# Optimization experiments

Measured on AMD Instinct MI355X. Metric: run time of the kernel, lower is better.

Reference implementation:

```python
import jax, jax.numpy as jnp
import numpy as np
import math

B, N, D, H, BS = 1, 2048, 1024, 16, 256  # batch, seq, d_model, heads, block_size


def setup_inputs() -> dict:
    key = jax.random.key(0)
    ks = jax.random.split(key, 8)
    s = 0.02  # init scale for projection weights
    return {
        "x": jax.random.normal(ks[0], (B, N, D), jnp.float32),
        "distance_bias": jax.random.uniform(ks[1], (N, N), dtype=jnp.float32),
        "Wq": jax.random.normal(ks[2], (D, D), jnp.float32) * s,
        "bq": jnp.zeros((D,), jnp.float32),
        "Wk": jax.random.normal(ks[3], (D, D), jnp.float32) * s,
        "bk": jnp.zeros((D,), jnp.float32),
        "Wv": jax.random.normal(ks[4], (D, D), jnp.float32) * s,
        "bv": jnp.zeros((D,), jnp.float32),
        "Wo": jax.random.normal(ks[5], (D, D), jnp.float32) * s,
        "bo": jnp.zeros((D,), jnp.float32),
    }


def reference(x, distance_bias, Wq, bq, Wk, bk, Wv, bv, Wo, bo):
    Bm, Nm, Dm = x.shape
    dk = Dm // H
    scale = 1.0 / math.sqrt(dk)
    nb = Nm // BS  # number of blocks along sequence

    def proj(W, b):
        # torch Linear: x @ W.T + b, then split heads -> [B, H, N, dk]
        return (x @ W.T + b).reshape(Bm, Nm, H, dk).transpose(0, 2, 1, 3)

    Q, K, V = proj(Wq, bq), proj(Wk, bk), proj(Wv, bv)

    # scores with toroidal bias subtracted (matches `scores - bias_block`)
    scores = jnp.einsum('bhqd,bhkd->bhqk', Q, K) * scale - distance_bias[None, None]
    # view as [B, H, n_qblk, BS, n_kblk, BS] and softmax PER (q-block, k-block)
    s6 = scores.reshape(Bm, H, nb, BS, nb, BS)
    w = jax.nn.softmax(s6, axis=-1)  # softmax over keys within each kv block

    Vb = V.reshape(Bm, H, nb, BS, dk)
    # sum over all kv blocks of (per-block softmax) @ V_block
    num = jnp.einsum('bhqsnk,bhnkd->bhqsd', w, Vb)  # [B,H,nb,BS,dk]
    # accumulated normalizer = sum of per-block softmax weights over all kv blocks
    norm = jnp.sum(w, axis=(4, 5))  # [B,H,nb,BS]
    O = num / (norm[..., None] + 1e-8)

    O = O.reshape(Bm, H, Nm, dk).transpose(0, 2, 1, 3).reshape(Bm, Nm, Dm)
    return O @ Wo.T + bo
```

## Files before the change

kernel.cpp:

```cpp
#include <hip/hip_runtime.h>
#include <hip/hip_fp16.h>

typedef _Float16 half8 __attribute__((ext_vector_type(8)));
typedef _Float16 half4v __attribute__((ext_vector_type(4)));
typedef float f32x4 __attribute__((ext_vector_type(4)));

#define NSEQ 2048
#define DMOD 1024
#define NHEAD 16
#define DK 64

#define GLOAD_LDS16(gp, lp) __builtin_amdgcn_global_load_lds(                 \
    (const __attribute__((address_space(1))) void*)(gp),                      \
    (__attribute__((address_space(3))) void*)(lp), 16, 0, 0)

#define WAIT_VM(n) (0xF70 | (n))


__global__ __launch_bounds__(256) void cast_pack(
    const float* __restrict__ x, const float* __restrict__ wq,
    const float* __restrict__ wk, const float* __restrict__ wv,
    const float* __restrict__ wo, const float* __restrict__ db,
    _Float16* __restrict__ dst, _Float16* __restrict__ bh)
{
    const int w = blockIdx.x * 4 + (threadIdx.x >> 6);
    const int ln = threadIdx.x & 63, m = ln & 15, qd = ln >> 4;
    if (w >= 12288) {
        const int loc = w - 12288;
        const float* p = db + (size_t)loc * 512 + ln * 8;
        float4 a = *(const float4*)p, b = *(const float4*)(p + 4);
        half8 h;
        h[0] = (_Float16)a.x; h[1] = (_Float16)a.y; h[2] = (_Float16)a.z; h[3] = (_Float16)a.w;
        h[4] = (_Float16)b.x; h[5] = (_Float16)b.y; h[6] = (_Float16)b.z; h[7] = (_Float16)b.w;
        *(half8*)(bh + (size_t)loc * 512 + ln * 8) = h;
        return;
    }
    const float* src; _Float16* d; int loc;
    if (w < 4096) { src = x; d = dst; loc = w; }
    else {
        const int w2 = w - 4096, mat = w2 >> 11;
        loc = w2 & 2047;
        src = mat == 0 ? wq : mat == 1 ? wk : mat == 2 ? wv : wo;
        d = dst + 2097152 + mat * 1048576;
    }
    const int st = loc >> 5, kc = loc & 31;
    const float* p = src + (size_t)(st * 16 + m) * 1024 + kc * 32 + qd * 8;
    float4 a = *(const float4*)p, b = *(const float4*)(p + 4);
    half8 h;
    h[0] = (_Float16)a.x; h[1] = (_Float16)a.y; h[2] = (_Float16)a.z; h[3] = (_Float16)a.w;
    h[4] = (_Float16)b.x; h[5] = (_Float16)b.y; h[6] = (_Float16)b.z; h[7] = (_Float16)b.w;
    *(half8*)(d + (size_t)(loc * 64 + ln) * 8) = h;
}

__global__ __launch_bounds__(256) void cvt_bias(
    const float* __restrict__ src, _Float16* __restrict__ dst)
{
    int i = (blockIdx.x * 256 + threadIdx.x) * 4;
    float4 v = *(const float4*)(src + i);
    half4v h;
    h[0] = (_Float16)v.x; h[1] = (_Float16)v.y;
    h[2] = (_Float16)v.z; h[3] = (_Float16)v.w;
    *(half4v*)(dst + i) = h;
}

template<int BM, int BN, int MODE>
__global__ __launch_bounds__(256) void tgemm(
    const _Float16* __restrict__ A, const _Float16* __restrict__ A2,
    const _Float16* __restrict__ W0, const _Float16* __restrict__ W1,
    const _Float16* __restrict__ W2,
    const float* __restrict__ b0, const float* __restrict__ b1,
    const float* __restrict__ b2,
    _Float16* __restrict__ oQ, _Float16* __restrict__ oK,
    _Float16* __restrict__ oV, float* __restrict__ oF)
{
    constexpr int MT = BM / 32, NT = BN / 32;
    constexpr int NA = BM / 64, NB = BN / 64;
    constexpr int SDMA = (MODE == 1 ? 2 * NA : NA) + NB;
    __shared__ _Float16 sA[3 * BM * 32];
    __shared__ _Float16 sA2[MODE == 1 ? 3 * BM * 32 : 1];
    __shared__ _Float16 sB[3 * BN * 32];
    const int tid = threadIdx.x, wv = tid >> 6, ln = tid & 63;
    const int m = ln & 15, qd = ln >> 4;
    const int row0 = blockIdx.x * BM;

    int sel = 0, colbase;
    const _Float16* W; const float* bias;
    if constexpr (MODE == 0) {
        sel = blockIdx.y >> 3;
        colbase = (blockIdx.y & 7) * BN;
        W = sel == 0 ? W0 : sel == 1 ? W1 : W2;
        bias = sel == 0 ? b0 : sel == 1 ? b1 : b2;
    } else {
        colbase = blockIdx.y * BN;
        W = W0; bias = b0;
    }
    const int wr = wv >> 1, wc = wv & 1;

    f32x4 acc[MT][NT];
#pragma unroll
    for (int i = 0; i < MT; ++i)
#pragma unroll
        for (int j = 0; j < NT; ++j) acc[i][j] = (f32x4){0.f, 0.f, 0.f, 0.f};

    auto stage = [&](int kc, int b) {
        _Float16* dA = sA + b * (BM * 32);
        _Float16* dB = sB + b * (BN * 32);
#pragma unroll
        for (int ra = 0; ra < NA; ++ra) {
            const int st = ra * 4 + wv;
            GLOAD_LDS16(A + ((size_t)((row0 >> 4) + st) * 32 + kc) * 512 + ln * 8,
                        dA + st * 512);
            if constexpr (MODE == 1) {
                _Float16* dA2 = sA2 + b * (BM * 32);
                GLOAD_LDS16(A2 + ((size_t)((row0 >> 4) + st) * 32 + kc) * 512 + ln * 8,
                            dA2 + st * 512);
            }
        }
#pragma unroll
        for (int rb = 0; rb < NB; ++rb) {
            const int st = rb * 4 + wv;
            GLOAD_LDS16(W + ((size_t)((colbase >> 4) + st) * 32 + kc) * 512 + ln * 8,
                        dB + st * 512);
        }
    };
    auto step = [&](int b) {
        const _Float16* cA = sA + b * (BM * 32);
        const _Float16* cB = sB + b * (BN * 32);
        half8 af[MT], bf[NT];
#pragma unroll
        for (int i = 0; i < MT; ++i) {
            const int off = ((wr * MT + i) * 64 + ln) * 8;
            if constexpr (MODE == 1) {
                const _Float16* cA2 = sA2 + b * (BM * 32);
                half8 xv = *(const half8*)(cA + off);
                half8 yv = *(const half8*)(cA2 + off);
                half8 f;
#pragma unroll
                for (int j = 0; j < 8; ++j)
                    f[j] = (_Float16)((float)xv[j] + (float)yv[j]);
                af[i] = f;
            } else {
                af[i] = *(const half8*)(cA + off);
            }
        }
#pragma unroll
        for (int j = 0; j < NT; ++j)
            bf[j] = *(const half8*)(cB + ((wc * NT + j) * 64 + ln) * 8);
#pragma unroll
        for (int i = 0; i < MT; ++i)
#pragma unroll
            for (int j = 0; j < NT; ++j)
                acc[i][j] = __builtin_amdgcn_mfma_f32_16x16x32_f16(af[i], bf[j], acc[i][j], 0, 0, 0);
    };

    stage(0, 0);
    stage(1, 1);
#pragma unroll
    for (int kc = 0; kc < 31; ++kc) {
        __builtin_amdgcn_s_waitcnt(WAIT_VM(SDMA));
        __builtin_amdgcn_s_barrier();
        if (kc < 30) stage(kc + 2, (kc + 2) % 3);
        step(kc % 3);
    }
    __builtin_amdgcn_s_waitcnt(WAIT_VM(0));
    __builtin_amdgcn_s_barrier();
    step(1);

#pragma unroll
    for (int j = 0; j < NT; ++j) {
        const int col = colbase + wc * (BN / 2) + j * 16 + m;
        const float bv = bias[col];
#pragma unroll
        for (int i = 0; i < MT; ++i) {
            const int crow0 = row0 + wr * (BM / 2) + i * 16 + qd * 4;
            if constexpr (MODE == 1) {
#pragma unroll
                for (int r = 0; r < 4; ++r)
                    oF[(size_t)(crow0 + r) * DMOD + col] = acc[i][j][r] + bv;
            } else {
                const int h = col >> 6, d = col & 63;
                if (sel == 0) {
#pragma unroll
                    for (int r = 0; r < 4; ++r)
                        oQ[h * (NSEQ * DK) + (crow0 + r) * DK + d] =
                            (_Float16)((acc[i][j][r] + bv) * 0.125f);
                } else if (sel == 1) {
#pragma unroll
                    for (int r = 0; r < 4; ++r) {
                        const int n = crow0 + r;
                        oK[(size_t)(((h * 16 + (n >> 7)) * 16
                                     + ((n >> 4) & 7) * 2 + (d >> 5)) * 64
                                    + (n & 15) + 16 * ((d >> 3) & 3)) * 8
                           + (d & 7)] = (_Float16)(acc[i][j][r] + bv);
                    }
                } else {
                    half4v hv;
#pragma unroll
                    for (int r = 0; r < 4; ++r) hv[r] = (_Float16)(acc[i][j][r] + bv);
                    const int n0 = crow0;
                    *(half4v*)(oV + (size_t)(((h * 16 + (n0 >> 7)) * 16
                                              + ((n0 >> 5) & 3) * 4 + ((d >> 4) & 3)) * 64
                                             + (d & 15) + 16 * ((n0 >> 3) & 3)) * 8
                               + (n0 & 7)) = hv;
                }
            }
        }
    }
}

__global__ __launch_bounds__(512, 4) void attn(
    const _Float16* __restrict__ Q, const _Float16* __restrict__ Kt,
    const _Float16* __restrict__ Vt, const _Float16* __restrict__ bias_h,
    _Float16* __restrict__ Op)
{
    __shared__ _Float16 sK[8192];
    __shared__ _Float16 sV[8192];
    __shared__ _Float16 sP[16384];
    const int tid = threadIdx.x, wv = tid >> 6, ln = tid & 63;
    const int m = ln & 15, qd = ln >> 4;
    const int h = blockIdx.x;
    const int q0 = blockIdx.y * 128 + wv * 16;
    const int kvb = blockIdx.z * 8;
    const _Float16* Qh = Q + h * (NSEQ * DK);
    const _Float16* Kh = Kt + h * (NSEQ * DK) + kvb * 8192;
    const _Float16* Vh = Vt + h * (NSEQ * DK) + kvb * 8192;
    const _Float16* brow = bias_h + (size_t)(q0 + m) * NSEQ + kvb * 128;

    half8 qf[2];
    qf[0] = *(const half8*)(Qh + (q0 + m) * DK + qd * 8);
    qf[1] = *(const half8*)(Qh + (q0 + m) * DK + 32 + qd * 8);

    f32x4 oacc[4], oU[4];
#pragma unroll
    for (int v = 0; v < 4; ++v) {
        oacc[v] = (f32x4){0.f, 0.f, 0.f, 0.f};
        oU[v]   = (f32x4){0.f, 0.f, 0.f, 0.f};
    }
    float bsum = 0.f;

    for (int ls = 0; ls < 8; ++ls) {
        if (ls) __syncthreads();
        GLOAD_LDS16(Kh + ls * 8192 + wv * 512 + ln * 8, sK + wv * 512);
        GLOAD_LDS16(Kh + ls * 8192 + (wv + 8) * 512 + ln * 8, sK + (wv + 8) * 512);
        GLOAD_LDS16(Vh + ls * 8192 + wv * 512 + ln * 8, sV + wv * 512);
        GLOAD_LDS16(Vh + ls * 8192 + (wv + 8) * 512 + ln * 8, sV + (wv + 8) * 512);
        half4v bcur[8];
#pragma unroll
        for (int t = 0; t < 8; ++t)
            bcur[t] = *(const half4v*)(brow + ls * 128 + t * 16 + qd * 4);
        __syncthreads();

#pragma unroll
        for (int t = 0; t < 8; ++t) {
            half8 kf0 = *(const half8*)(sK + ((t * 2 + 0) * 64 + ln) * 8);
            half8 kf1 = *(const half8*)(sK + ((t * 2 + 1) * 64 + ln) * 8);
            f32x4 s = {0.f, 0.f, 0.f, 0.f};
            s = __builtin_amdgcn_mfma_f32_16x16x32_f16(kf0, qf[0], s, 0, 0, 0);
            s = __builtin_amdgcn_mfma_f32_16x16x32_f16(kf1, qf[1], s, 0, 0, 0);
            float p0 = __expf(s[0] - (float)bcur[t][0]);
            float p1 = __expf(s[1] - (float)bcur[t][1]);
            float p2 = __expf(s[2] - (float)bcur[t][2]);
            float p3 = __expf(s[3] - (float)bcur[t][3]);
            bsum += (p0 + p1) + (p2 + p3);
            half4v ph;
            ph[0] = (_Float16)p0; ph[1] = (_Float16)p1;
            ph[2] = (_Float16)p2; ph[3] = (_Float16)p3;
            *(half4v*)(sP + wv * 2048 + (t >> 1) * 512
                       + (((t & 1) * 2 + (qd >> 1)) * 16 + m) * 8
                       + (qd & 1) * 4) = ph;
        }

#pragma unroll
        for (int kk = 0; kk < 4; ++kk) {
            half8 pa = *(const half8*)(sP + wv * 2048 + kk * 512 + ln * 8);
#pragma unroll
            for (int vt = 0; vt < 4; ++vt) {
                half8 vb = *(const half8*)(sV + ((kk * 4 + vt) * 64 + ln) * 8);
                oU[vt] = __builtin_amdgcn_mfma_f32_16x16x32_f16(pa, vb, oU[vt], 0, 0, 0);
            }
        }

        if (ls & 1) {
            float s2 = bsum;
            s2 += __shfl_xor(s2, 16, 64);
            s2 += __shfl_xor(s2, 32, 64);
            float inv = 1.0f / (8.0f * s2);
            float iv[4];
#pragma unroll
            for (int r = 0; r < 4; ++r) iv[r] = __shfl(inv, qd * 4 + r, 64);
#pragma unroll
            for (int vt = 0; vt < 4; ++vt) {
#pragma unroll
                for (int r = 0; r < 4; ++r) oacc[vt][r] += iv[r] * oU[vt][r];
                oU[vt] = (f32x4){0.f, 0.f, 0.f, 0.f};
            }
            bsum = 0.f;
        }
    }

    _Float16* Opz = Op + (size_t)blockIdx.z * 2097152;
    const int st = blockIdx.y * 8 + wv;
#pragma unroll
    for (int vt = 0; vt < 4; ++vt) {
        const int d = h * 64 + vt * 16 + m;
        _Float16* base = Opz + (size_t)(st * 32 + (d >> 5)) * 512
                         + ((d >> 3) & 3) * 128 + (d & 7);
#pragma unroll
        for (int r = 0; r < 4; ++r)
            base[(qd * 4 + r) * 8] = (_Float16)oacc[vt][r];
    }
}

extern "C" void kernel_launch(void* const* d_in, const int* in_sizes, int n_in,
                              void* d_out, int out_size, void* d_ws, size_t ws_size,
                              hipStream_t stream)
{
    const float* x  = (const float*)d_in[0];
    const float* db = (const float*)d_in[1];
    const float* Wq = (const float*)d_in[2];
    const float* bq = (const float*)d_in[3];
    const float* Wk = (const float*)d_in[4];
    const float* bk = (const float*)d_in[5];
    const float* Wv = (const float*)d_in[6];
    const float* bv = (const float*)d_in[7];
    const float* Wo = (const float*)d_in[8];
    const float* bo = (const float*)d_in[9];
    float* out = (float*)d_out;

    _Float16* ws  = (_Float16*)d_ws;
    _Float16* xh  = ws;
    _Float16* wqh = xh  + 2097152;
    _Float16* wkh = wqh + 1048576;
    _Float16* wvh = wkh + 1048576;
    _Float16* woh = wvh + 1048576;
    _Float16* Qb  = woh + 1048576;
    _Float16* Kb  = Qb  + 2097152;
    _Float16* Vtb = Kb  + 2097152;
    _Float16* Oh0 = Vtb + 2097152;
    _Float16* Oh1 = Oh0 + 2097152;

    const bool big_ws = ws_size >= (size_t)41943040;
    _Float16* bh = big_ws ? (Oh1 + 2097152) : ws;

    cast_pack<<<big_ws ? 5120 : 3072, 256, 0, stream>>>(
        x, Wq, Wk, Wv, Wo, db, xh, bh);

    tgemm<64, 128, 0><<<dim3(32, 24), 256, 0, stream>>>(
        xh, nullptr, wqh, wkh, wvh, bq, bk, bv, Qb, Kb, Vtb, nullptr);

    if (!big_ws)
        cvt_bias<<<4096, 256, 0, stream>>>(db, bh);

    attn<<<dim3(NHEAD, NSEQ / 128, 2), 512, 0, stream>>>(Qb, Kb, Vtb, bh, Oh0);

    tgemm<64, 128, 1><<<dim3(32, 8), 256, 0, stream>>>(
        Oh0, Oh1, woh, nullptr, nullptr, bo, nullptr, nullptr,
        nullptr, nullptr, nullptr, out);
}
```

Measured before the change: 180.5 us.

## Switch tgemm to double-buffered BK=64 stages and shrink output GEMM tile

The GEMM pipeline moves from a 3-stage ring of K=32 chunks to a 2-stage double buffer of K=64 chunks. This halves the number of barrier/wait iterations per K loop and doubles the MFMA work between syncs. The output projection GEMM also switches to a 64x64 tile on a 32x16 grid to put more blocks on the GPU. The trade-off is one less stage of prefetch depth, so load latency may be less well hidden, and the extra barrier per iteration adds some sync cost.

Measured after the change: 169.1 us. 1.07x faster.

```diff
diff --git a/kernel.cpp b/kernel.cpp
--- a/kernel.cpp
+++ b/kernel.cpp
@@ -63,7 +63,7 @@
     *(half4v*)(dst + i) = h;
 }
 
-template<int BM, int BN, int MODE>
+template<int BM, int BN, int BK, int MODE>
 __global__ __launch_bounds__(256) void tgemm(
     const _Float16* __restrict__ A, const _Float16* __restrict__ A2,
     const _Float16* __restrict__ W0, const _Float16* __restrict__ W1,
@@ -74,11 +74,13 @@
     _Float16* __restrict__ oV, float* __restrict__ oF)
 {
     constexpr int MT = BM / 32, NT = BN / 32;
-    constexpr int NA = BM / 64, NB = BN / 64;
-    constexpr int SDMA = (MODE == 1 ? 2 * NA : NA) + NB;
-    __shared__ _Float16 sA[3 * BM * 32];
-    __shared__ _Float16 sA2[MODE == 1 ? 3 * BM * 32 : 1];
-    __shared__ _Float16 sB[3 * BN * 32];
+    constexpr int KC = BK / 32;
+    constexpr int NSTEP = 1024 / BK;
+    constexpr int NAc = BM / 64, NBc = BN / 64;
+    constexpr int SDMA = KC * ((MODE == 1 ? 2 * NAc : NAc) + NBc);
+    __shared__ _Float16 sA[2 * BM * BK];
+    __shared__ _Float16 sA2[MODE == 1 ? 2 * BM * BK : 1];
+    __shared__ _Float16 sB[2 * BN * BK];
     const int tid = threadIdx.x, wv = tid >> 6, ln = tid & 63;
     const int m = ln & 15, qd = ln >> 4;
     const int row0 = blockIdx.x * BM;
@@ -102,69 +104,77 @@
 #pragma unroll
         for (int j = 0; j < NT; ++j) acc[i][j] = (f32x4){0.f, 0.f, 0.f, 0.f};
 
-    auto stage = [&](int kc, int b) {
-        _Float16* dA = sA + b * (BM * 32);
-        _Float16* dB = sB + b * (BN * 32);
-#pragma unroll
-        for (int ra = 0; ra < NA; ++ra) {
-            const int st = ra * 4 + wv;
-            GLOAD_LDS16(A + ((size_t)((row0 >> 4) + st) * 32 + kc) * 512 + ln * 8,
-                        dA + st * 512);
-            if constexpr (MODE == 1) {
-                _Float16* dA2 = sA2 + b * (BM * 32);
-                GLOAD_LDS16(A2 + ((size_t)((row0 >> 4) + st) * 32 + kc) * 512 + ln * 8,
-                            dA2 + st * 512);
-            }
-        }
-#pragma unroll
-        for (int rb = 0; rb < NB; ++rb) {
-            const int st = rb * 4 + wv;
-            GLOAD_LDS16(W + ((size_t)((colbase >> 4) + st) * 32 + kc) * 512 + ln * 8,
-                        dB + st * 512);
+    auto stage = [&](int s, int b) {
+        _Float16* dA = sA + b * (BM * BK);
+        _Float16* dB = sB + b * (BN * BK);
+#pragma unroll
+        for (int c = 0; c < KC; ++c) {
+            const int kc = s * KC + c;
+#pragma unroll
+            for (int ra = 0; ra < NAc; ++ra) {
+                const int st = ra * 4 + wv;
+                GLOAD_LDS16(A + ((size_t)((row0 >> 4) + st) * 32 + kc) * 512 + ln * 8,
+                            dA + (c * (BM / 16) + st) * 512);
+                if constexpr (MODE == 1) {
+                    _Float16* dA2 = sA2 + b * (BM * BK);
+                    GLOAD_LDS16(A2 + ((size_t)((row0 >> 4) + st) * 32 + kc) * 512 + ln * 8,
+                                dA2 + (c * (BM / 16) + st) * 512);
+                }
+            }
+#pragma unroll
+            for (int rb = 0; rb < NBc; ++rb) {
+                const int st = rb * 4 + wv;
+                GLOAD_LDS16(W + ((size_t)((colbase >> 4) + st) * 32 + kc) * 512 + ln * 8,
+                            dB + (c * (BN / 16) + st) * 512);
+            }
         }
     };
     auto step = [&](int b) {
-        const _Float16* cA = sA + b * (BM * 32);
-        const _Float16* cB = sB + b * (BN * 32);
-        half8 af[MT], bf[NT];
-#pragma unroll
-        for (int i = 0; i < MT; ++i) {
-            const int off = ((wr * MT + i) * 64 + ln) * 8;
-            if constexpr (MODE == 1) {
-                const _Float16* cA2 = sA2 + b * (BM * 32);
-                half8 xv = *(const half8*)(cA + off);
-                half8 yv = *(const half8*)(cA2 + off);
-                half8 f;
-#pragma unroll
-                for (int j = 0; j < 8; ++j)
-                    f[j] = (_Float16)((float)xv[j] + (float)yv[j]);
-                af[i] = f;
-            } else {
-                af[i] = *(const half8*)(cA + off);
-            }
-        }
-#pragma unroll
-        for (int j = 0; j < NT; ++j)
-            bf[j] = *(const half8*)(cB + ((wc * NT + j) * 64 + ln) * 8);
-#pragma unroll
-        for (int i = 0; i < MT; ++i)
+#pragma unroll
+        for (int c = 0; c < KC; ++c) {
+            const _Float16* cA = sA + b * (BM * BK) + c * (BM * 32);
+            const _Float16* cB = sB + b * (BN * BK) + c * (BN * 32);
+            half8 af[MT], bf[NT];
+#pragma unroll
+            for (int i = 0; i < MT; ++i) {
+                const int off = ((wr * MT + i) * 64 + ln) * 8;
+                if constexpr (MODE == 1) {
+                    const _Float16* cA2 = sA2 + b * (BM * BK) + c * (BM * 32);
+                    half8 xv = *(const half8*)(cA + off);
+                    half8 yv = *(const half8*)(cA2 + off);
+                    half8 f;
+#pragma unroll
+                    for (int j = 0; j < 8; ++j)
+                        f[j] = (_Float16)((float)xv[j] + (float)yv[j]);
+                    af[i] = f;
+                } else {
+                    af[i] = *(const half8*)(cA + off);
+                }
+            }
 #pragma unroll
             for (int j = 0; j < NT; ++j)
-                acc[i][j] = __builtin_amdgcn_mfma_f32_16x16x32_f16(af[i], bf[j], acc[i][j], 0, 0, 0);
+                bf[j] = *(const half8*)(cB + ((wc * NT + j) * 64 + ln) * 8);
+#pragma unroll
+            for (int i = 0; i < MT; ++i)
+#pragma unroll
+                for (int j = 0; j < NT; ++j)
+                    acc[i][j] = __builtin_amdgcn_mfma_f32_16x16x32_f16(af[i], bf[j], acc[i][j], 0, 0, 0);
+        }
     };
 
     stage(0, 0);
-    stage(1, 1);
-#pragma unroll
-    for (int kc = 0; kc < 31; ++kc) {
-        __builtin_amdgcn_s_waitcnt(WAIT_VM(SDMA));
+#pragma unroll
+    for (int s = 0; s < NSTEP; ++s) {
+        if (s) __builtin_amdgcn_s_barrier();
+        if (s + 1 < NSTEP) {
+            stage(s + 1, (s + 1) & 1);
+            __builtin_amdgcn_s_waitcnt(WAIT_VM(SDMA));
+        } else {
+            __builtin_amdgcn_s_waitcnt(WAIT_VM(0));
+        }
         __builtin_amdgcn_s_barrier();
-        if (kc < 30) stage(kc + 2, (kc + 2) % 3);
-        step(kc % 3);
-    }
-    __builtin_amdgcn_s_waitcnt(WAIT_VM(0));
-    __builtin_amdgcn_s_barrier();
-    step(1);
+        step(s & 1);
+    }
 
 #pragma unroll
     for (int j = 0; j < NT; ++j) {
@@ -345,7 +355,7 @@
     cast_pack<<<big_ws ? 5120 : 3072, 256, 0, stream>>>(
         x, Wq, Wk, Wv, Wo, db, xh, bh);
 
-    tgemm<64, 128, 0><<<dim3(32, 24), 256, 0, stream>>>(
+    tgemm<64, 128, 64, 0><<<dim3(32, 24), 256, 0, stream>>>(
         xh, nullptr, wqh, wkh, wvh, bq, bk, bv, Qb, Kb, Vtb, nullptr);
 
     if (!big_ws)
@@ -353,7 +363,7 @@
 
     attn<<<dim3(NHEAD, NSEQ / 128, 2), 512, 0, stream>>>(Qb, Kb, Vtb, bh, Oh0);
 
-    tgemm<64, 128, 1><<<dim3(32, 8), 256, 0, stream>>>(
+    tgemm<64, 64, 64, 1><<<dim3(32, 16), 256, 0, stream>>>(
         Oh0, Oh1, woh, nullptr, nullptr, bo, nullptr, nullptr,
         nullptr, nullptr, nullptr, out);
 }
```
